# Performance work log

Measured on AMD Instinct MI355X. Metric: run time of the kernel, lower is better.

Reference implementation:

```python
import jax, jax.numpy as jnp
import numpy as np

N, IN_DIM, HID, HEADS = 20000, 3000, 128, 4
S_DIM, P_DIM = 32, 32
E = 320000
NEG_SLOPE = 0.2
ETA = 1e-6


def _glorot(key, shape):
    fan_in, fan_out = shape[0], shape[-1] if len(shape) > 1 else shape[0]
    lim = np.sqrt(6.0 / (fan_in + fan_out))
    return jax.random.uniform(key, shape, jnp.float32, -lim, lim)


def _gat_params(key, in_dim, out_ch, heads, concat):
    k1, k2, k3 = jax.random.split(key, 3)
    Wl = _glorot(k1, (in_dim, heads * out_ch))
    Wr = _glorot(k2, (in_dim, heads * out_ch))
    att = _glorot(k3, (heads, out_ch))
    b = jnp.zeros((heads * out_ch,) if concat else (out_ch,), jnp.float32)
    return Wl, Wr, att, b


def setup_inputs() -> dict:
    key = jax.random.key(0)
    ks = jax.random.split(key, 6)
    x = jax.random.normal(ks[0], (N, IN_DIM), jnp.float32)
    edge_index = jax.random.randint(ks[1], (2, E), 0, N, jnp.int32)
    out = {"x": x, "edge_index": edge_index}
    for name, kk, (ind, oc, h, cc) in [
        ("s1", ks[2], (IN_DIM, HID, HEADS, True)),
        ("s2", ks[3], (HID * HEADS, S_DIM * 2, 1, False)),
        ("p1", ks[4], (IN_DIM, HID, HEADS, True)),
        ("p2", ks[5], (HID * HEADS, P_DIM * 2, 1, False)),
    ]:
        Wl, Wr, att, b = _gat_params(kk, ind, oc, h, cc)
        out[f"Wl_{name}"] = Wl
        out[f"Wr_{name}"] = Wr
        out[f"att_{name}"] = att
        out[f"b_{name}"] = b
    return out


def gatv2(x, src, dst, Wl, Wr, att, b, heads, out_ch, concat):
    n = x.shape[0]
    xl = (x @ Wl).reshape(n, heads, out_ch)  # source transform
    xr = (x @ Wr).reshape(n, heads, out_ch)  # target transform
    m = xl[src]                                           # [E, H, C] messages
    e = jnp.sum(att * jax.nn.leaky_relu(m + xr[dst], NEG_SLOPE), axis=-1)  # [E, H]
    emax = jax.ops.segment_max(e, dst, num_segments=n)    # self-loops -> no empty segments
    ee = jnp.exp(e - emax[dst])
    denom = jax.ops.segment_sum(ee, dst, num_segments=n)
    alpha = ee / denom[dst]                               # segment softmax over incoming edges
    agg = jax.ops.segment_sum(m * alpha[..., None], dst, num_segments=n)  # [N, H, C]
    out = agg.reshape(n, heads * out_ch) if concat else agg.mean(axis=1)
    return out + b


def reference(x, edge_index, Wl_s1, Wr_s1, att_s1, b_s1, Wl_s2, Wr_s2, att_s2, b_s2,
              Wl_p1, Wr_p1, att_p1, b_p1, Wl_p2, Wr_p2, att_p2, b_p2):
    n = x.shape[0]
    loop = jnp.arange(n, dtype=edge_index.dtype)
    src = jnp.concatenate([edge_index[0], loop])  # add_self_loops (PyG default)
    dst = jnp.concatenate([edge_index[1], loop])
    s = jax.nn.relu(gatv2(x, src, dst, Wl_s1, Wr_s1, att_s1, b_s1, HEADS, HID, True))
    s = gatv2(s, src, dst, Wl_s2, Wr_s2, att_s2, b_s2, 1, S_DIM * 2, False)
    p = gatv2(x, src, dst, Wl_p1, Wr_p1, att_p1, b_p1, HEADS, HID, True)
    p = gatv2(p, src, dst, Wl_p2, Wr_p2, att_p2, b_p2, 1, P_DIM * 2, False)
    mu = jnp.concatenate([s[:, :S_DIM], p[:, :P_DIM]], axis=-1)
    sig = jnp.concatenate([jax.nn.softplus(s[:, S_DIM:]) + ETA,
                           jax.nn.softplus(p[:, P_DIM:]) + ETA], axis=-1)
    return mu, sig
```

## Files before the change

kernel.cpp:

```cpp
#include <hip/hip_runtime.h>
#include <cstdint>

#define NN     20000
#define NE     320000
#define ETOT   340000
#define K1R    3000
#define K1     3072
#define NPAD   20224
#define NCOL1  2048
#define LDA2   1024
#define MU_SZ  1280000

typedef __bf16 bf16x8 __attribute__((ext_vector_type(8)));
typedef float f32x4 __attribute__((ext_vector_type(4)));
typedef unsigned short u16x8 __attribute__((ext_vector_type(8)));

__device__ inline unsigned short f2bf(float f) {
  union { float f; unsigned u; } v; v.f = f;
  unsigned r = v.u + 0x7FFFu + ((v.u >> 16) & 1u);
  return (unsigned short)(r >> 16);
}
__device__ inline float bf2f(unsigned short h) {
  union { unsigned u; float f; } v; v.u = ((unsigned)h) << 16;
  return v.f;
}

typedef const __attribute__((address_space(1))) void* gas1_t;
typedef __attribute__((address_space(3))) void* las3_t;
__device__ inline void llds16(const void* g, void* l) {
  __builtin_amdgcn_global_load_lds((gas1_t)(uintptr_t)g,
                                   (las3_t)(uint32_t)(uintptr_t)l, 16, 0, 0);
}


__global__ __launch_bounds__(256)
void k_convert_x(const float* __restrict__ X, unsigned short* __restrict__ Xb) {
  const int CH = K1 / 8;
  int idx = blockIdx.x * 256 + threadIdx.x;
  if (idx >= NPAD * CH) return;
  int r = idx / CH, c8 = (idx % CH) * 8;
  u16x8 o;
  if (r < NN && c8 < K1R) {
    const float4* p = (const float4*)(X + (size_t)r * K1R + c8);
    float4 a = p[0], b = p[1];
    o[0]=f2bf(a.x); o[1]=f2bf(a.y); o[2]=f2bf(a.z); o[3]=f2bf(a.w);
    o[4]=f2bf(b.x); o[5]=f2bf(b.y); o[6]=f2bf(b.z); o[7]=f2bf(b.w);
  } else {
#pragma unroll
    for (int j = 0; j < 8; j++) o[j] = 0;
  }
  *(u16x8*)(Xb + (size_t)r * K1 + c8) = o;
}

__global__ __launch_bounds__(256)
void k_pack_w1(const float* __restrict__ W0, const float* __restrict__ W1,
               const float* __restrict__ W2, const float* __restrict__ W3,
               unsigned short* __restrict__ Wp) {
  __shared__ float tile[64][65];
  int k0 = blockIdx.x * 64, n0 = blockIdx.y * 64;
  int m = n0 >> 9, c0 = n0 & 511;
  const float* W = (m == 0) ? W0 : (m == 1) ? W1 : (m == 2) ? W2 : W3;
  int tx = threadIdx.x & 63, ty = threadIdx.x >> 6;
#pragma unroll
  for (int rep = 0; rep < 16; rep++) {
    int i = ty + rep * 4;
    int k = k0 + i;
    tile[i][tx] = (k < K1R) ? W[(size_t)k * 512 + c0 + tx] : 0.f;
  }
  __syncthreads();
#pragma unroll
  for (int rep = 0; rep < 16; rep++) {
    int i = ty + rep * 4;
    Wp[(size_t)(n0 + i) * K1 + k0 + tx] = f2bf(tile[tx][i]);
  }
}

__global__ __launch_bounds__(256)
void k_pack_w2(const float* __restrict__ Wl, const float* __restrict__ Wr,
               unsigned short* __restrict__ B2) {
  int idx = blockIdx.x * 256 + threadIdx.x;
  if (idx >= 128 * 1024) return;
  int n = idx >> 10, k = idx & 1023, kk = k & 511;
  float v = (n < 64) ? Wl[(size_t)kk * 64 + n] : Wr[(size_t)kk * 64 + (n - 64)];
  B2[idx] = f2bf(v);
}


__global__ __launch_bounds__(256)
void k_count(const int* __restrict__ ei, int* __restrict__ counts) {
  int e = blockIdx.x * 256 + threadIdx.x;
  if (e >= ETOT) return;
  int dst = (e < NE) ? ei[NE + e] : (e - NE);
  atomicAdd(&counts[dst], 1);
}

__global__ void k_scan(const int* __restrict__ counts, int* __restrict__ row_ptr) {
  __shared__ int part[1024];
  int t = threadIdx.x;
  int base = t * 20;
  int loc[20];
  int s = 0;
#pragma unroll
  for (int i = 0; i < 20; i++) {
    int idx = base + i;
    loc[i] = s;
    s += (idx < NN) ? counts[idx] : 0;
  }
  part[t] = s;
  __syncthreads();
  for (int off = 1; off < 1024; off <<= 1) {
    int v = (t >= off) ? part[t - off] : 0;
    __syncthreads();
    part[t] += v;
    __syncthreads();
  }
  int pre = (t > 0) ? part[t - 1] : 0;
#pragma unroll
  for (int i = 0; i < 20; i++) {
    int idx = base + i;
    if (idx <= NN) row_ptr[idx] = pre + loc[i];
  }
}

__global__ __launch_bounds__(256)
void k_scatter(const int* __restrict__ ei, const int* __restrict__ row_ptr,
               int* __restrict__ fill, int* __restrict__ csr_src) {
  int e = blockIdx.x * 256 + threadIdx.x;
  if (e >= ETOT) return;
  int s_, d_;
  if (e < NE) { s_ = ei[e]; d_ = ei[NE + e]; } else { s_ = d_ = e - NE; }
  int pos = row_ptr[d_] + atomicAdd(&fill[d_], 1);
  csr_src[pos] = s_;
}


#define NT1 48

#define STAGE_ONE do { \
  if (sctr < 4 * NT1) { \
    int ts_ = sctr >> 2, o_ = sctr & 3, sb_ = ts_ & 1; \
    const unsigned short* gb_; char* lb_; int rb_; \
    if (o_ == 0)      { gb_ = A; rb_ = bmBase;       lb_ = lds + (sb_*2+0)*16384; } \
    else if (o_ == 1) { gb_ = B; rb_ = bnBase;       lb_ = lds + 65536 + (sb_*2+0)*16384; } \
    else if (o_ == 2) { gb_ = B; rb_ = bnBase + 128; lb_ = lds + 65536 + (sb_*2+1)*16384; } \
    else              { gb_ = A; rb_ = bmBase + 128; lb_ = lds + (sb_*2+1)*16384; } \
    const unsigned short* g0_ = gb_ + (size_t)(rb_ + trow) * 3072 + ts_ * 64 + scol; \
    llds16(g0_, lb_ + wid * 1024); \
    llds16(g0_ + (size_t)64 * 3072, lb_ + 8192 + wid * 1024); \
    sctr++; \
  } \
} while (0)

#define RDA(DST, BASE) do { \
  _Pragma("unroll") \
  for (int mi = 0; mi < 2; mi++) { \
    int r_ = rw * 32 + mi * 16 + l15; \
    DST[0][mi] = *(const bf16x8*)((BASE) + r_ * 128 + sw0); \
    DST[1][mi] = *(const bf16x8*)((BASE) + r_ * 128 + sw1); \
  } \
} while (0)

#define RDB(DST, BASE) do { \
  _Pragma("unroll") \
  for (int ni = 0; ni < 4; ni++) { \
    int r_ = cw * 64 + ni * 16 + l15; \
    DST[0][ni] = *(const bf16x8*)((BASE) + r_ * 128 + sw0); \
    DST[1][ni] = *(const bf16x8*)((BASE) + r_ * 128 + sw1); \
  } \
} while (0)

#define MF(MH, NH, AV, BV) do { \
  _Pragma("unroll") \
  for (int mi = 0; mi < 2; mi++) \
    _Pragma("unroll") \
    for (int ni = 0; ni < 4; ni++) { \
      acc[MH][NH][mi][ni] = __builtin_amdgcn_mfma_f32_16x16x32_bf16(AV[0][mi], BV[0][ni], acc[MH][NH][mi][ni], 0, 0, 0); \
      acc[MH][NH][mi][ni] = __builtin_amdgcn_mfma_f32_16x16x32_bf16(AV[1][mi], BV[1][ni], acc[MH][NH][mi][ni], 0, 0, 0); \
    } \
} while (0)

__global__ __launch_bounds__(512, 2)
void gemm256(const unsigned short* __restrict__ A, const unsigned short* __restrict__ B,
             unsigned short* __restrict__ C) {
  __shared__ char lds[131072];
  int tid = threadIdx.x, wid = tid >> 6, lane = tid & 63;
  int l15 = lane & 15;
  int rw = wid & 3, cw = wid >> 2;
  int bid = blockIdx.x;
  int swz = (bid & 7) * 79 + (bid >> 3);
  int bm = swz % 79, bn = swz / 79;
  int bmBase = bm * 256, bnBase = bn * 256;
  int trow = tid >> 3;
  int scol = ((tid & 7) ^ ((tid >> 3) & 7)) * 8;
  int sw0 = (((lane >> 4) + 0) ^ (lane & 7)) * 16;
  int sw1 = (((lane >> 4) + 4) ^ (lane & 7)) * 16;
  f32x4 acc[2][2][2][4] = {};

  int sctr = 0;
  for (int i = 0; i < 4; i++) STAGE_ONE;
  asm volatile("s_waitcnt vmcnt(0)" ::: "memory");
  __builtin_amdgcn_s_barrier();
  asm volatile("" ::: "memory");

  for (int t = 0; t < NT1; t++) {
    int buf = t & 1;
    STAGE_ONE; STAGE_ONE; STAGE_ONE; STAGE_ONE;
    const char* A0h = lds + (buf * 2 + 0) * 16384;
    const char* A1h = lds + (buf * 2 + 1) * 16384;
    const char* B0h = lds + 65536 + (buf * 2 + 0) * 16384;
    const char* B1h = lds + 65536 + (buf * 2 + 1) * 16384;
    bf16x8 a0[2][2], a1[2][2], b0[2][4], b1[2][4];
    RDA(a0, A0h); RDA(a1, A1h);
    RDB(b0, B0h); RDB(b1, B1h);
    asm volatile("" ::: "memory");
    __builtin_amdgcn_s_setprio(1);
    MF(0, 0, a0, b0);
    MF(1, 0, a1, b0);
    MF(1, 1, a1, b1);
    MF(0, 1, a0, b1);
    __builtin_amdgcn_s_setprio(0);
    asm volatile("s_waitcnt vmcnt(0)" ::: "memory");
    __builtin_amdgcn_s_barrier();
    asm volatile("" ::: "memory");
  }

  unsigned short (*sq)[128] = (unsigned short (*)[128])lds;
#pragma unroll
  for (int mh = 0; mh < 2; mh++)
#pragma unroll
    for (int nh = 0; nh < 2; nh++) {
      __syncthreads();
#pragma unroll
      for (int mi = 0; mi < 2; mi++)
#pragma unroll
        for (int ni = 0; ni < 4; ni++)
#pragma unroll
          for (int r = 0; r < 4; r++)
            sq[rw * 32 + mi * 16 + (lane >> 4) * 4 + r][cw * 64 + ni * 16 + l15] =
                f2bf(acc[mh][nh][mi][ni][r]);
      __syncthreads();
#pragma unroll
      for (int it = 0; it < 4; it++) {
        int idx = it * 512 + tid;
        int row = idx >> 4, ch = idx & 15;
        *(u16x8*)(C + (size_t)(bmBase + mh * 128 + row) * NCOL1 + bnBase + nh * 128 + ch * 8) =
            *(const u16x8*)&sq[row][ch * 8];
      }
    }
}


__global__ __launch_bounds__(256)
void gemm_l2(const unsigned short* __restrict__ As, const unsigned short* __restrict__ Bs,
             float* __restrict__ Cs,
             const unsigned short* __restrict__ Ap, const unsigned short* __restrict__ Bp,
             float* __restrict__ Cp) {
  const int K = LDA2, lda = LDA2, ldb = LDA2, ldc = 128, mreal = NN;
  const unsigned short* A = blockIdx.y ? Ap : As;
  const unsigned short* B = blockIdx.y ? Bp : Bs;
  float* C = blockIdx.y ? Cp : Cs;
  __shared__ char smem_raw[16384];
  unsigned short* sA = (unsigned short*)smem_raw;
  unsigned short* sB = sA + 128 * 32;
  int bm = blockIdx.x;
  int tid = threadIdx.x, wid = tid >> 6, lane = tid & 63;
  int wr = wid >> 1, wc = wid & 1;
  f32x4 acc[4][4] = {};

  int ar = 32 * wid + (lane >> 2);
  int acol = (lane & 3) * 8;
  const unsigned short* Ag = A + (size_t)(bm * 128 + ar) * lda + acol;
  const unsigned short* Bg = B + (size_t)ar * ldb + acol;
  unsigned short* la0 = sA + (wid * 2) * 512;
  unsigned short* lb0 = sB + (wid * 2) * 512;
  int frow = lane & 15, koff = (lane >> 4) * 8;

  for (int kt = 0; kt < K; kt += 32) {
    llds16(Ag + kt, la0);
    llds16(Ag + kt + (size_t)16 * lda, la0 + 512);
    llds16(Bg + kt, lb0);
    llds16(Bg + kt + (size_t)16 * ldb, lb0 + 512);
    __syncthreads();
    bf16x8 af[4], bfr[4];
#pragma unroll
    for (int mi = 0; mi < 4; mi++)
      af[mi] = *(const bf16x8*)(sA + (wr * 64 + mi * 16 + frow) * 32 + koff);
#pragma unroll
    for (int ni = 0; ni < 4; ni++)
      bfr[ni] = *(const bf16x8*)(sB + (wc * 64 + ni * 16 + frow) * 32 + koff);
#pragma unroll
    for (int mi = 0; mi < 4; mi++)
#pragma unroll
      for (int ni = 0; ni < 4; ni++)
        acc[mi][ni] = __builtin_amdgcn_mfma_f32_16x16x32_bf16(af[mi], bfr[ni], acc[mi][ni], 0, 0, 0);
    __syncthreads();
  }

#pragma unroll
  for (int mi = 0; mi < 4; mi++) {
    int grow0 = bm * 128 + wr * 64 + mi * 16 + (lane >> 4) * 4;
#pragma unroll
    for (int ni = 0; ni < 4; ni++) {
      int gcol = wc * 64 + ni * 16 + (lane & 15);
#pragma unroll
      for (int r = 0; r < 4; r++) {
        int grow = grow0 + r;
        if (grow < mreal) C[(size_t)grow * ldc + gcol] = acc[mi][ni][r];
      }
    }
  }
}


__global__ __launch_bounds__(256)
void edge_agg1(const unsigned short* __restrict__ XL1,
               const int* __restrict__ row_ptr, const int* __restrict__ csr_src,
               const float* __restrict__ att_s, const float* __restrict__ att_p,
               const float* __restrict__ b_s, const float* __restrict__ b_p,
               unsigned short* __restrict__ A2s, unsigned short* __restrict__ A2p) {
  int gw = (blockIdx.x * 256 + threadIdx.x) >> 6;
  if (gw >= NN * 2) return;
  int n = gw >> 1, br = gw & 1;
  int lane = threadIdx.x & 63;
  int cb = lane * 8;
  const float* att = br ? att_p : att_s;
  const float* bias = br ? b_p : b_s;
  float xr[8], at[8], agg[8];
  bf16x8 xrv = *(const bf16x8*)(XL1 + (size_t)n * NCOL1 + br * 1024 + 512 + cb);
#pragma unroll
  for (int j = 0; j < 8; j++) { xr[j] = (float)xrv[j]; at[j] = att[cb + j]; agg[j] = 0.f; }
  float M = -1e30f, S = 0.f;
  const size_t srcoff = (size_t)br * 1024 + cb;
  int pe = row_ptr[n + 1];
  for (int p = row_ptr[n]; p < pe; ++p) {
    int src = csr_src[p];
    bf16x8 mv = *(const bf16x8*)(XL1 + (size_t)src * NCOL1 + srcoff);
    float mj[8], part = 0.f;
#pragma unroll
    for (int j = 0; j < 8; j++) {
      mj[j] = (float)mv[j];
      float t = mj[j] + xr[j];
      t = (t > 0.f) ? t : 0.2f * t;
      part = fmaf(at[j], t, part);
    }
#pragma unroll
    for (int w = 1; w < 16; w <<= 1) part += __shfl_xor(part, w);
    float nm = fmaxf(M, part);
    float fac = __expf(M - nm);
    float wgt = __expf(part - nm);
    S = S * fac + wgt;
#pragma unroll
    for (int j = 0; j < 8; j++) agg[j] = agg[j] * fac + wgt * mj[j];
    M = nm;
  }
  float inv = 1.f / S;
  u16x8 hv, lv;
  unsigned short* A2 = br ? A2p : A2s;
#pragma unroll
  for (int j = 0; j < 8; j++) {
    float v = agg[j] * inv + bias[cb + j];
    if (!br) v = fmaxf(v, 0.f);
    unsigned short h = f2bf(v);
    float lo = v - bf2f(h);
    hv[j] = h; lv[j] = f2bf(lo);
  }
  *(u16x8*)(A2 + (size_t)n * LDA2 + cb) = hv;
  *(u16x8*)(A2 + (size_t)n * LDA2 + 512 + cb) = lv;
}


__global__ __launch_bounds__(256)
void edge_agg2(const float* __restrict__ C2s, const float* __restrict__ C2p,
               const int* __restrict__ row_ptr, const int* __restrict__ csr_src,
               const float* __restrict__ att_s, const float* __restrict__ att_p,
               const float* __restrict__ b_s, const float* __restrict__ b_p,
               float* __restrict__ out) {
  int gw = (blockIdx.x * 256 + threadIdx.x) >> 6;
  if (gw >= NN * 2) return;
  int n = gw >> 1, br = gw & 1;
  int lane = threadIdx.x & 63;
  const float* C2 = br ? C2p : C2s;
  float xr = C2[(size_t)n * 128 + 64 + lane];
  float at = (br ? att_p : att_s)[lane];
  float M = -1e30f, S = 0.f, agg = 0.f;
  int pe = row_ptr[n + 1];
  for (int p = row_ptr[n]; p < pe; ++p) {
    int src = csr_src[p];
    float m = C2[(size_t)src * 128 + lane];
    float t = m + xr;
    t = (t > 0.f) ? t : 0.2f * t;
    float part = at * t;
#pragma unroll
    for (int w = 1; w < 64; w <<= 1) part += __shfl_xor(part, w);
    float nm = fmaxf(M, part);
    float fac = __expf(M - nm);
    float wgt = __expf(part - nm);
    S = S * fac + wgt;
    agg = agg * fac + wgt * m;
    M = nm;
  }
  float v = agg / S + (br ? b_p : b_s)[lane];
  if (lane < 32) {
    out[(size_t)n * 64 + br * 32 + lane] = v;
  } else {
    float sp = fmaxf(v, 0.f) + log1pf(__expf(-fabsf(v))) + 1e-6f;
    out[(size_t)MU_SZ + n * 64 + br * 32 + (lane - 32)] = sp;
  }
}


extern "C" void kernel_launch(void* const* d_in, const int* in_sizes, int n_in,
                              void* d_out, int out_size, void* d_ws, size_t ws_size,
                              hipStream_t stream) {
  const float* x      = (const float*)d_in[0];
  const int*   ei     = (const int*)d_in[1];
  const float* Wl_s1  = (const float*)d_in[2];
  const float* Wr_s1  = (const float*)d_in[3];
  const float* att_s1 = (const float*)d_in[4];
  const float* b_s1   = (const float*)d_in[5];
  const float* Wl_s2  = (const float*)d_in[6];
  const float* Wr_s2  = (const float*)d_in[7];
  const float* att_s2 = (const float*)d_in[8];
  const float* b_s2   = (const float*)d_in[9];
  const float* Wl_p1  = (const float*)d_in[10];
  const float* Wr_p1  = (const float*)d_in[11];
  const float* att_p1 = (const float*)d_in[12];
  const float* b_p1   = (const float*)d_in[13];
  const float* Wl_p2  = (const float*)d_in[14];
  const float* Wr_p2  = (const float*)d_in[15];
  const float* att_p2 = (const float*)d_in[16];
  const float* b_p2   = (const float*)d_in[17];

  char* ws = (char*)d_ws;
  unsigned short* Xb   = (unsigned short*)(ws + 0);
  unsigned short* A2s  = (unsigned short*)(ws + 0);
  unsigned short* A2p  = (unsigned short*)(ws + 41156608);
  float*          C2s  = (float*)(ws + 82313216);
  float*          C2p  = (float*)(ws + 92553216);
  unsigned short* B2s  = (unsigned short*)(ws + 102793216);
  unsigned short* B2p  = (unsigned short*)(ws + 103055360);
  unsigned short* Wp   = (unsigned short*)(ws + 124256256);
  unsigned short* XL1  = (unsigned short*)(ws + 136839168);
  int* counts  = (int*)(ws + 219676672);
  int* fill    = (int*)(ws + 219756672);
  int* row_ptr = (int*)(ws + 219836672);
  int* csr_src = (int*)(ws + 219916688);

  hipMemsetAsync(counts, 0, NN * sizeof(int), stream);
  hipMemsetAsync(fill, 0, NN * sizeof(int), stream);

  k_convert_x<<<30336, 256, 0, stream>>>(x, Xb);
  k_pack_w1<<<dim3(48, 32), 256, 0, stream>>>(Wl_s1, Wr_s1, Wl_p1, Wr_p1, Wp);
  k_count<<<(ETOT + 255) / 256, 256, 0, stream>>>(ei, counts);
  k_scan<<<1, 1024, 0, stream>>>(counts, row_ptr);
  k_scatter<<<(ETOT + 255) / 256, 256, 0, stream>>>(ei, row_ptr, fill, csr_src);

  gemm256<<<632, 512, 0, stream>>>(Xb, Wp, XL1);

  k_pack_w2<<<512, 256, 0, stream>>>(Wl_s2, Wr_s2, B2s);
  k_pack_w2<<<512, 256, 0, stream>>>(Wl_p2, Wr_p2, B2p);

  edge_agg1<<<10000, 256, 0, stream>>>(XL1, row_ptr, csr_src, att_s1, att_p1, b_s1, b_p1, A2s, A2p);

  gemm_l2<<<dim3(157, 2), 256, 0, stream>>>(A2s, B2s, C2s, A2p, B2p, C2p);

  edge_agg2<<<10000, 256, 0, stream>>>(C2s, C2p, row_ptr, csr_src, att_s2, att_p2, b_s2, b_p2, (float*)d_out);
}
```

Before: 631.6 us.

## Interleave global-to-LDS staging with MFMA phases and stagger warp roles

The main GEMM loop now alternates the four staging loads with LDS fragment reads and MFMA quadrants instead of issuing all loads up front. Half the waves process the quadrants in the opposite order, and the staging order is changed to match. The aim is to spread memory and LDS traffic across the compute phases and reduce bank and port contention. The block-to-tile swizzle is also replaced by a plain mapping (bn = bid&7), which may change L2 reuse. Per-quadrant setprio toggling is added as well.

```diff
diff --git a/kernel.cpp b/kernel.cpp
--- a/kernel.cpp
+++ b/kernel.cpp
@@ -138,12 +138,12 @@
 
 #define STAGE_ONE do { \
   if (sctr < 4 * NT1) { \
-    int ts_ = sctr >> 2, o_ = sctr & 3, sb_ = ts_ & 1; \
+    int ts_ = sctr >> 2, u_ = sctr & 3, sb_ = ts_ & 1; \
     const unsigned short* gb_; char* lb_; int rb_; \
-    if (o_ == 0)      { gb_ = A; rb_ = bmBase;       lb_ = lds + (sb_*2+0)*16384; } \
-    else if (o_ == 1) { gb_ = B; rb_ = bnBase;       lb_ = lds + 65536 + (sb_*2+0)*16384; } \
-    else if (o_ == 2) { gb_ = B; rb_ = bnBase + 128; lb_ = lds + 65536 + (sb_*2+1)*16384; } \
-    else              { gb_ = A; rb_ = bmBase + 128; lb_ = lds + (sb_*2+1)*16384; } \
+    if (u_ == 0)      { gb_ = A; rb_ = bmBase + 128; lb_ = lds + (sb_*2+1)*16384; } \
+    else if (u_ == 1) { gb_ = B; rb_ = bnBase + 128; lb_ = lds + 65536 + (sb_*2+1)*16384; } \
+    else if (u_ == 2) { gb_ = B; rb_ = bnBase;       lb_ = lds + 65536 + (sb_*2+0)*16384; } \
+    else              { gb_ = A; rb_ = bmBase;       lb_ = lds + (sb_*2+0)*16384; } \
     const unsigned short* g0_ = gb_ + (size_t)(rb_ + trow) * 3072 + ts_ * 64 + scol; \
     llds16(g0_, lb_ + wid * 1024); \
     llds16(g0_ + (size_t)64 * 3072, lb_ + 8192 + wid * 1024); \
@@ -170,6 +170,7 @@
 } while (0)
 
 #define MF(MH, NH, AV, BV) do { \
+  __builtin_amdgcn_s_setprio(1); \
   _Pragma("unroll") \
   for (int mi = 0; mi < 2; mi++) \
     _Pragma("unroll") \
@@ -177,6 +178,7 @@
       acc[MH][NH][mi][ni] = __builtin_amdgcn_mfma_f32_16x16x32_bf16(AV[0][mi], BV[0][ni], acc[MH][NH][mi][ni], 0, 0, 0); \
       acc[MH][NH][mi][ni] = __builtin_amdgcn_mfma_f32_16x16x32_bf16(AV[1][mi], BV[1][ni], acc[MH][NH][mi][ni], 0, 0, 0); \
     } \
+  __builtin_amdgcn_s_setprio(0); \
 } while (0)
 
 __global__ __launch_bounds__(512, 2)
@@ -186,9 +188,9 @@
   int tid = threadIdx.x, wid = tid >> 6, lane = tid & 63;
   int l15 = lane & 15;
   int rw = wid & 3, cw = wid >> 2;
+  int role = (wid >> 2) & 1;
   int bid = blockIdx.x;
-  int swz = (bid & 7) * 79 + (bid >> 3);
-  int bm = swz % 79, bn = swz / 79;
+  int bn = bid & 7, bm = bid >> 3;
   int bmBase = bm * 256, bnBase = bn * 256;
   int trow = tid >> 3;
   int scol = ((tid & 7) ^ ((tid >> 3) & 7)) * 8;
@@ -204,21 +206,37 @@
 
   for (int t = 0; t < NT1; t++) {
     int buf = t & 1;
-    STAGE_ONE; STAGE_ONE; STAGE_ONE; STAGE_ONE;
     const char* A0h = lds + (buf * 2 + 0) * 16384;
     const char* A1h = lds + (buf * 2 + 1) * 16384;
     const char* B0h = lds + 65536 + (buf * 2 + 0) * 16384;
     const char* B1h = lds + 65536 + (buf * 2 + 1) * 16384;
     bf16x8 a0[2][2], a1[2][2], b0[2][4], b1[2][4];
-    RDA(a0, A0h); RDA(a1, A1h);
-    RDB(b0, B0h); RDB(b1, B1h);
-    asm volatile("" ::: "memory");
-    __builtin_amdgcn_s_setprio(1);
-    MF(0, 0, a0, b0);
-    MF(1, 0, a1, b0);
-    MF(1, 1, a1, b1);
-    MF(0, 1, a0, b1);
-    __builtin_amdgcn_s_setprio(0);
+
+    if (role == 0) {
+      STAGE_ONE;
+      RDA(a0, A0h); RDB(b0, B0h);
+      MF(0, 0, a0, b0);
+      STAGE_ONE;
+      RDA(a1, A1h);
+      MF(1, 0, a1, b0);
+      STAGE_ONE;
+      RDB(b1, B1h);
+      MF(1, 1, a1, b1);
+      STAGE_ONE;
+      MF(0, 1, a0, b1);
+    } else {
+      STAGE_ONE;
+      RDA(a1, A1h); RDB(b1, B1h);
+      MF(1, 1, a1, b1);
+      STAGE_ONE;
+      RDA(a0, A0h);
+      MF(0, 1, a0, b1);
+      STAGE_ONE;
+      RDB(b0, B0h);
+      MF(0, 0, a0, b0);
+      STAGE_ONE;
+      MF(1, 0, a1, b0);
+    }
     asm volatile("s_waitcnt vmcnt(0)" ::: "memory");
     __builtin_amdgcn_s_barrier();
     asm volatile("" ::: "memory");
```

New measurement: 627.7 us. No clear change (-0.6%).
